# Optimization experiments

Hardware: AMD Instinct MI355X
Metric: run time of the kernel (lower is better)

Reference implementation:

```python
import jax, jax.numpy as jnp
import numpy as np

N, E, F, H, G, EPS = 50000, 500000, 128, 192, 256, 1e-5


def setup_inputs() -> dict:
    key = jax.random.key(0)
    ks = jax.random.split(key, 16)
    s = 0.05
    return {
        "x": jax.random.normal(ks[0], (N, F), jnp.float32),
        "edge_index": jax.random.randint(ks[1], (2, E), 0, N),
        "batch": jnp.sort(jax.random.randint(ks[2], (N,), 0, G)),
        "num_graphs": G,
        "w_rel0": jax.random.normal(ks[3], (H, F)) * s,
        "b_rel0": jnp.zeros((H,), jnp.float32),
        "w_root0": jax.random.normal(ks[4], (H, F)) * s,
        "w_rel": jax.random.normal(ks[5], (3, H, H)) * s,
        "b_rel": jnp.zeros((3, H), jnp.float32),
        "w_root": jax.random.normal(ks[6], (3, H, H)) * s,
        "bn_gamma": jnp.ones((4, H), jnp.float32),
        "bn_beta": jnp.zeros((4, H), jnp.float32),
        "head_w1": jax.random.normal(ks[7], (H, H)) * s,
        "head_b1": jnp.zeros((H,), jnp.float32),
        "head_w2": jax.random.normal(ks[8], (H, H)) * s,
        "head_b2": jnp.zeros((H,), jnp.float32),
        "out_w": jax.random.normal(ks[9], (1, H)) * s,
        "out_b": jnpp if False else jnp.zeros((1,), jnp.float32),
    }


def _conv_bn_relu(x, src, dst, n_nodes, wr, br, wroot, gamma, beta):
    # PyG GraphConv: out_i = lin_rel(sum_{j->i} x_j) + lin_root(x_i)
    agg = jax.ops.segment_sum(x[src], dst, num_segments=n_nodes)  # [N, d]
    h = agg @ wr.T + br + x @ wroot.T                             # [N, H]
    mu = h.mean(axis=0)
    var = h.var(axis=0)  # biased, as torch BN train mode
    h = (h - mu) * jax.lax.rsqrt(var + EPS) * gamma + beta
    return jax.nn.relu(h)


def reference(x, edge_index, batch, num_graphs, w_rel0, b_rel0, w_root0,
              w_rel, b_rel, w_root, bn_gamma, bn_beta,
              head_w1, head_b1, head_w2, head_b2, out_w, out_b):
    src, dst = edge_index[0], edge_index[1]
    n_nodes = x.shape[0]
    h = _conv_bn_relu(x, src, dst, n_nodes, w_rel0, b_rel0, w_root0,
                      bn_gamma[0], bn_beta[0])
    for i in range(3):
        h = _conv_bn_relu(h, src, dst, n_nodes, w_rel[i], b_rel[i], w_root[i],
                          bn_gamma[i + 1], bn_beta[i + 1])
    # global mean pool per graph
    sums = jax.ops.segment_sum(h, batch, num_segments=num_graphs)   # [G, H]
    cnts = jax.ops.segment_sum(jnp.ones((n_nodes,), h.dtype), batch,
                               num_segments=num_graphs)
    g = sums / jnp.maximum(cnts, 1.0)[:, None]
    # MLP head (dropout = eval) + output linear
    hh = jax.nn.relu(g @ head_w1.T + head_b1) @ head_w2.T + head_b2
    out = hh @ out_w.T + out_b                                      # [G, 1]
    return out[:, 0]
```

## Files before the change

### kernel.cpp

```cpp
#include <hip/hip_runtime.h>

#define HD 192
#define FD0 128
#define NG 256
#define BNEPS 1e-5f

#define STAT_S  1048576.0f
#define STAT_IS (1.0f / 1048576.0f)
#define POOL_S  65536.0f
#define POOL_IS (1.0f / 65536.0f)

typedef unsigned short u16;
typedef __attribute__((ext_vector_type(8))) short bf16x8;
typedef __attribute__((ext_vector_type(4))) float f32x4;

static inline int idiv(int a, int b) { return (a + b - 1) / b; }

__device__ __forceinline__ float b2f(u16 u) {
    unsigned int v = ((unsigned int)u) << 16;
    return __builtin_bit_cast(float, v);
}
__device__ __forceinline__ u16 f2b(float f) {
    unsigned int x = __builtin_bit_cast(unsigned int, f);
    return (u16)((x + 0x7FFFu + ((x >> 16) & 1u)) >> 16);
}

__device__ __forceinline__ void bn_params(const long long* __restrict__ statsq,
    const float* __restrict__ gamma, const float* __restrict__ beta,
    int N, int c, float& sc, float& sh)
{
    const float inv = 1.0f / (float)N;
    const float sum = (float)statsq[c] * STAT_IS;
    const float sq  = (float)statsq[HD + c] * STAT_IS;
    const float mu  = sum * inv;
    const float var = sq * inv - mu * mu;
    const float s   = gamma[c] * rsqrtf(var + BNEPS);
    sc = s; sh = beta[c] - mu * s;
}

__device__ __forceinline__ void async_cp16(const void* g, void* l) {
    __builtin_amdgcn_global_load_lds(
        (const __attribute__((address_space(1))) unsigned int*)g,
        (__attribute__((address_space(3))) unsigned int*)l, 16, 0, 0);
}

__global__ __launch_bounds__(256) void convert_bf16(const float* __restrict__ in,
                                                    u16* __restrict__ out, int n4)
{
    const int i = blockIdx.x * 256 + threadIdx.x;
    if (i >= n4) return;
    const float4 v = ((const float4*)in)[i];
    u16 o[4] = { f2b(v.x), f2b(v.y), f2b(v.z), f2b(v.w) };
    ((ushort4*)out)[i] = *(ushort4*)o;
}

__device__ __forceinline__ void pack_one(const float* __restrict__ wr,
    const float* __restrict__ wt, u16* __restrict__ out, int K, int idx)
{
    const int j  = idx & 7;
    const int t  = idx >> 3;
    const int c  = t & 15;
    const int kg = (t >> 4) & 3;
    const int rest = t >> 6;
    const int fglob = rest % 12;
    const int chunk = rest / 12;
    const int col = fglob * 16 + c;
    const int k   = chunk * 32 + kg * 8 + j;
    const float v = (k < K) ? wr[(size_t)col * K + k] : wt[(size_t)col * K + (k - K)];
    out[idx] = f2b(v);
}

__global__ __launch_bounds__(256) void pack_fuse(const float* __restrict__ wr0,
    const float* __restrict__ wt0, const float* __restrict__ w_rel,
    const float* __restrict__ w_root, const float* __restrict__ hw1,
    const float* __restrict__ hw2, u16* __restrict__ wp0,
    u16* __restrict__ wp123, float* __restrict__ w1t, float* __restrict__ w2t)
{
    const int T0 = HD * 2 * FD0;
    const int T1 = HD * 2 * HD;
    const int TW = HD * HD;
    int idx = blockIdx.x * 256 + threadIdx.x;
    if (idx < T0) { pack_one(wr0, wt0, wp0, FD0, idx); return; }
    idx -= T0;
    if (idx < 3 * T1) {
        const int li = idx / T1;
        const int r  = idx - li * T1;
        pack_one(w_rel + (size_t)li * HD * HD, w_root + (size_t)li * HD * HD,
                 wp123 + (size_t)li * T1, HD, r);
        return;
    }
    idx -= 3 * T1;
    if (idx >= 2 * TW) return;
    const float* w = (idx < TW) ? hw1 : hw2;
    float*       o = (idx < TW) ? w1t : w2t;
    const int r = (idx < TW) ? idx : idx - TW;
    const int t = r % HD, k = r / HD;
    o[r] = w[(size_t)t * HD + k];
}

__global__ __launch_bounds__(256) void hist_kernel(const int* __restrict__ dst,
                                                   int* __restrict__ deg, int E)
{
    const int e = blockIdx.x * 256 + threadIdx.x;
    if (e < E) atomicAdd(&deg[dst[e]], 1);
}

__global__ __launch_bounds__(256) void scan_partial(const int* __restrict__ deg,
                                                    int* __restrict__ psum, int N)
{
    __shared__ int s[256];
    const int t = threadIdx.x;
    const int i = blockIdx.x * 256 + t;
    s[t] = (i < N) ? deg[i] : 0;
    __syncthreads();
    for (int off = 128; off > 0; off >>= 1) {
        if (t < off) s[t] += s[t + off];
        __syncthreads();
    }
    if (t == 0) psum[blockIdx.x] = s[0];
}

__global__ __launch_bounds__(256) void scan_small(int* __restrict__ psum, int M)
{
    __shared__ int s[256];
    const int t = threadIdx.x;
    s[t] = (t < M) ? psum[t] : 0;
    __syncthreads();
    for (int off = 1; off < 256; off <<= 1) {
        const int u = (t >= off) ? s[t - off] : 0;
        __syncthreads();
        s[t] += u;
        __syncthreads();
    }
    if (t < M) psum[t] = (t == 0) ? 0 : s[t - 1];
}

__global__ __launch_bounds__(256) void scan_expand(int* __restrict__ deg,
    const int* __restrict__ psum, int* __restrict__ rowptr, int N, int E)
{
    __shared__ int s[256];
    const int t = threadIdx.x;
    const int i = blockIdx.x * 256 + t;
    const int v = (i < N) ? deg[i] : 0;
    s[t] = v;
    __syncthreads();
    for (int off = 1; off < 256; off <<= 1) {
        const int u = (t >= off) ? s[t - off] : 0;
        __syncthreads();
        s[t] += u;
        __syncthreads();
    }
    if (i < N) {
        const int base = psum[blockIdx.x] + s[t] - v;
        rowptr[i] = base;
        deg[i]    = base;
    }
    if (i == N - 1) rowptr[N] = E;
}

__global__ __launch_bounds__(256) void fill_kernel(const int* __restrict__ src,
    const int* __restrict__ dst, int* __restrict__ cursor,
    int* __restrict__ eidx, int E)
{
    const int e = blockIdx.x * 256 + threadIdx.x;
    if (e >= E) return;
    const int p = atomicAdd(&cursor[dst[e]], 1);
    eidx[p] = src[e];
}

template<int FD, bool BN>
__global__ __launch_bounds__(256) void gather_kernel(
    const u16* __restrict__ hsrc, const int* __restrict__ rowptr,
    const int* __restrict__ eidx, u16* __restrict__ aggb, int N,
    const long long* __restrict__ statsq, const float* __restrict__ gamma,
    const float* __restrict__ beta)
{
    constexpr int OCT = FD / 8;
    __shared__ float scs[FD], shs[FD];
    const int t = threadIdx.x;
    if (BN) {
        if (t < FD) {
            float sc, sh;
            bn_params(statsq, gamma, beta, N, t, sc, sh);
            scs[t] = sc; shs[t] = sh;
        }
        __syncthreads();
    }
    const int lane = t & 63;
    const int half = lane >> 5;
    const int o    = lane & 31;
    const int n    = blockIdx.x * 4 + (t >> 6);
    if (n >= N) return;
    const bool act = (o < OCT);
    const int beg = rowptr[n], end = rowptr[n + 1];

    float scr[8], shr[8];
    if (BN && act) {
#pragma unroll
        for (int i = 0; i < 8; ++i) { scr[i] = scs[o * 8 + i]; shr[i] = shs[o * 8 + i]; }
    }

    float acc[8];
#pragma unroll
    for (int i = 0; i < 8; ++i) acc[i] = 0.f;

    auto consume = [&](uint4 v) {
        const u16* pu = (const u16*)&v;
#pragma unroll
        for (int i = 0; i < 8; ++i) {
            float f = b2f(pu[i]);
            if (BN) f = fmaxf(0.f, fmaf(f, scr[i], shr[i]));
            acc[i] += f;
        }
    };

    int j = beg + half;
    for (; j + 6 < end; j += 8) {
        const int s0 = eidx[j],     s1 = eidx[j + 2];
        const int s2 = eidx[j + 4], s3 = eidx[j + 6];
        if (act) {
            const uint4 v0 = *(const uint4*)(hsrc + (size_t)s0 * FD + o * 8);
            const uint4 v1 = *(const uint4*)(hsrc + (size_t)s1 * FD + o * 8);
            const uint4 v2 = *(const uint4*)(hsrc + (size_t)s2 * FD + o * 8);
            const uint4 v3 = *(const uint4*)(hsrc + (size_t)s3 * FD + o * 8);
            consume(v0); consume(v1); consume(v2); consume(v3);
        }
    }
    for (; j < end; j += 2) {
        const int s0 = eidx[j];
        if (act) consume(*(const uint4*)(hsrc + (size_t)s0 * FD + o * 8));
    }
#pragma unroll
    for (int i = 0; i < 8; ++i) acc[i] += __shfl_xor(acc[i], 32);

    if (half == 0 && act) {
        u16 ov[8];
#pragma unroll
        for (int i = 0; i < 8; ++i) ov[i] = f2b(acc[i]);
        *(uint4*)(aggb + (size_t)n * FD + o * 8) = *(uint4*)ov;
    }
}

template<int K1, int K2, bool BN>
__global__ __launch_bounds__(512, 1) void gemm_mfma(
    const u16* __restrict__ A1, const u16* A2,
    const u16* __restrict__ Wb, const float* __restrict__ bias,
    u16* Hout, long long* __restrict__ statsq_out,
    const long long* __restrict__ statsq_in, const float* __restrict__ gamma,
    const float* __restrict__ beta, int N)
{
    constexpr int KC  = K1 + K2;
    constexpr int NC  = KC / 32;
    constexpr int NC1 = K1 / 32;
    __shared__ u16 bsh[HD * KC];
    __shared__ float scs[K2], shs[K2];

    const int tid  = threadIdx.x;
    const int wave = tid >> 6, lane = tid & 63;
    const int c = lane & 15, kg = lane >> 4;
    const int row0 = blockIdx.x * 256 + wave * 32;

    {
        constexpr int NST = (HD * KC) / (512 * 8);
        const u16* wsrc = Wb + tid * 8;
        u16* ldst = bsh + tid * 8;
#pragma unroll
        for (int i = 0; i < NST; ++i)
            async_cp16(wsrc + i * 4096, ldst + i * 4096);
    }
    if (BN) {
        if (tid < K2) {
            float sc, sh;
            bn_params(statsq_in, gamma, beta, N, tid, sc, sh);
            scs[tid] = sc; shs[tid] = sh;
        }
    }

    int arc[2];
#pragma unroll
    for (int m = 0; m < 2; ++m) {
        const int r = row0 + m * 16 + c;
        arc[m] = r < N ? r : N - 1;
    }

    f32x4 acc[2][12];
#pragma unroll
    for (int m = 0; m < 2; ++m)
#pragma unroll
        for (int f = 0; f < 12; ++f) acc[m][f] = (f32x4){0.f, 0.f, 0.f, 0.f};

    auto aload = [&](int ch, bf16x8* d) {
#pragma unroll
        for (int m = 0; m < 2; ++m) {
            const u16* p = (ch < NC1)
                ? (A1 + (size_t)arc[m] * K1 + ch * 32 + kg * 8)
                : (A2 + (size_t)arc[m] * K2 + (ch - NC1) * 32 + kg * 8);
            d[m] = *(const bf16x8*)p;
        }
    };

    bf16x8 ring[4][2];
#pragma unroll
    for (int p = 0; p < 4; ++p)
        if (p < NC) aload(p, ring[p]);

    __syncthreads();

#pragma unroll
    for (int ch = 0; ch < NC; ++ch) {
        bf16x8 a[2] = { ring[ch & 3][0], ring[ch & 3][1] };
        if (ch + 4 < NC) aload(ch + 4, ring[ch & 3]);
        if (BN && ch >= NC1) {
            const int k0 = (ch - NC1) * 32 + kg * 8;
            const float4 s0 = *(const float4*)&scs[k0];
            const float4 s1 = *(const float4*)&scs[k0 + 4];
            const float4 h0 = *(const float4*)&shs[k0];
            const float4 h1 = *(const float4*)&shs[k0 + 4];
            const float scv[8] = {s0.x,s0.y,s0.z,s0.w,s1.x,s1.y,s1.z,s1.w};
            const float shv[8] = {h0.x,h0.y,h0.z,h0.w,h1.x,h1.y,h1.z,h1.w};
#pragma unroll
            for (int m = 0; m < 2; ++m) {
                const u16* pa = (const u16*)&a[m];
                u16 tv[8];
#pragma unroll
                for (int i = 0; i < 8; ++i)
                    tv[i] = f2b(fmaxf(0.f, fmaf(b2f(pa[i]), scv[i], shv[i])));
                a[m] = *(bf16x8*)tv;
            }
        }
#pragma unroll
        for (int f = 0; f < 12; ++f) {
            const bf16x8 b = *(const bf16x8*)&bsh[ch * 6144 + f * 512 + kg * 128 + c * 8];
            acc[0][f] = __builtin_amdgcn_mfma_f32_16x16x32_bf16(a[0], b, acc[0][f], 0, 0, 0);
            acc[1][f] = __builtin_amdgcn_mfma_f32_16x16x32_bf16(a[1], b, acc[1][f], 0, 0, 0);
        }
    }

    float s1v[12], s2v[12];
#pragma unroll
    for (int f = 0; f < 12; ++f) { s1v[f] = 0.f; s2v[f] = 0.f; }

#pragma unroll
    for (int f = 0; f < 12; ++f) {
        const int col = f * 16 + c;
        const float bv = bias[col];
#pragma unroll
        for (int m = 0; m < 2; ++m)
#pragma unroll
            for (int r = 0; r < 4; ++r) {
                const int orow = row0 + m * 16 + kg * 4 + r;
                if (orow < N) {
                    const float v = acc[m][f][r] + bv;
                    s1v[f] += v;
                    s2v[f] += v * v;
                    Hout[(size_t)orow * HD + col] = f2b(v);
                }
            }
    }
#pragma unroll
    for (int f = 0; f < 12; ++f) {
        s1v[f] += __shfl_xor(s1v[f], 16); s1v[f] += __shfl_xor(s1v[f], 32);
        s2v[f] += __shfl_xor(s2v[f], 16); s2v[f] += __shfl_xor(s2v[f], 32);
    }
    __syncthreads();
    float* red = (float*)bsh;
    if (kg == 0) {
#pragma unroll
        for (int f = 0; f < 12; ++f) {
            red[wave * HD + f * 16 + c]            = s1v[f];
            red[8 * HD + wave * HD + f * 16 + c]   = s2v[f];
        }
    }
    __syncthreads();
    if (tid < HD) {
        float a1 = 0.f, a2 = 0.f;
#pragma unroll
        for (int w = 0; w < 8; ++w) {
            a1 += red[w * HD + tid];
            a2 += red[8 * HD + w * HD + tid];
        }
        atomicAdd((unsigned long long*)&statsq_out[tid],
                  (unsigned long long)(long long)llrintf(a1 * STAT_S));
        atomicAdd((unsigned long long*)&statsq_out[HD + tid],
                  (unsigned long long)(long long)llrintf(a2 * STAT_S));
    }
}

__global__ __launch_bounds__(192) void pool_partial(const u16* __restrict__ h,
    const int* __restrict__ batch, int* __restrict__ gsumq, int N,
    const long long* __restrict__ statsq, const float* __restrict__ gamma,
    const float* __restrict__ beta)
{
    __shared__ float scs[HD], shs[HD];
    const int t = threadIdx.x;
    {
        float sc, sh;
        bn_params(statsq, gamma, beta, N, t, sc, sh);
        scs[t] = sc; shs[t] = sh;
    }
    __syncthreads();
    const int rl  = t / 24;
    const int oct = t % 24;
    const int r0  = blockIdx.x * 256;
    const int rend = (r0 + 256 < N) ? r0 + 256 : N;

    float scr[8], shr[8];
#pragma unroll
    for (int i = 0; i < 8; ++i) { scr[i] = scs[oct * 8 + i]; shr[i] = shs[oct * 8 + i]; }

    float facc[8];
#pragma unroll
    for (int i = 0; i < 8; ++i) facc[i] = 0.f;
    int cur = -1;

    for (int r = r0 + rl; r < rend; r += 8) {
        const int b = batch[r];
        if (b != cur) {
            if (cur >= 0) {
                int* q = gsumq + (size_t)cur * HD + oct * 8;
#pragma unroll
                for (int i = 0; i < 8; ++i)
                    atomicAdd(&q[i], __float2int_rn(facc[i] * POOL_S));
            }
#pragma unroll
            for (int i = 0; i < 8; ++i) facc[i] = 0.f;
            cur = b;
        }
        const uint4 pv = *(const uint4*)(h + (size_t)r * HD + oct * 8);
        const u16* pu = (const u16*)&pv;
#pragma unroll
        for (int i = 0; i < 8; ++i)
            facc[i] += fmaxf(0.f, fmaf(b2f(pu[i]), scr[i], shr[i]));
    }
    if (cur >= 0) {
        int* q = gsumq + (size_t)cur * HD + oct * 8;
#pragma unroll
        for (int i = 0; i < 8; ++i)
            atomicAdd(&q[i], __float2int_rn(facc[i] * POOL_S));
    }
}

__global__ __launch_bounds__(192) void head_kernel(
    const int* __restrict__ gsumq, const int* __restrict__ batch, int N,
    const float* __restrict__ w1t, const float* __restrict__ b1,
    const float* __restrict__ w2t, const float* __restrict__ b2,
    const float* __restrict__ ow, const float* __restrict__ ob,
    float* __restrict__ out)
{
    __shared__ float gv[HD];
    __shared__ float h1[HD];
    __shared__ float h2[HD];
    const int g = blockIdx.x;
    const int t = threadIdx.x;

    int lo = 0, hi = N;
    while (lo < hi) { int m = (lo + hi) >> 1; if (batch[m] < g) lo = m + 1; else hi = m; }
    const int start = lo;
    hi = N;
    while (lo < hi) { int m = (lo + hi) >> 1; if (batch[m] < g + 1) lo = m + 1; else hi = m; }
    const int end = lo;
    const float cnt = fmaxf((float)(end - start), 1.0f);

    gv[t] = (float)gsumq[(size_t)g * HD + t] * POOL_IS / cnt;
    __syncthreads();
    {
        float acc = b1[t];
#pragma unroll 4
        for (int k = 0; k < HD; ++k)
            acc = fmaf(gv[k], w1t[k * HD + t], acc);
        h1[t] = fmaxf(acc, 0.f);
    }
    __syncthreads();
    {
        float acc = b2[t];
#pragma unroll 4
        for (int k = 0; k < HD; ++k)
            acc = fmaf(h1[k], w2t[k * HD + t], acc);
        h2[t] = acc * ow[t];
    }
    __syncthreads();
    if (t < 64) {
        float s = h2[t] + h2[t + 64] + h2[t + 128];
#pragma unroll
        for (int d = 1; d < 64; d <<= 1) s += __shfl_xor(s, d);
        if (t == 0) out[g] = s + ob[0];
    }
}

extern "C" void kernel_launch(void* const* d_in, const int* in_sizes, int n_in,
                              void* d_out, int out_size, void* d_ws, size_t ws_size,
                              hipStream_t stream)
{
    const float* x       = (const float*)d_in[0];
    const int*   ei      = (const int*)d_in[1];
    const int*   batch   = (const int*)d_in[2];
    const float* w_rel0  = (const float*)d_in[4];
    const float* b_rel0  = (const float*)d_in[5];
    const float* w_root0 = (const float*)d_in[6];
    const float* w_rel   = (const float*)d_in[7];
    const float* b_rel   = (const float*)d_in[8];
    const float* w_root  = (const float*)d_in[9];
    const float* bn_g    = (const float*)d_in[10];
    const float* bn_b    = (const float*)d_in[11];
    const float* hw1     = (const float*)d_in[12];
    const float* hb1     = (const float*)d_in[13];
    const float* hw2     = (const float*)d_in[14];
    const float* hb2     = (const float*)d_in[15];
    const float* ow      = (const float*)d_in[16];
    const float* ob      = (const float*)d_in[17];
    float* out = (float*)d_out;

    const int N = in_sizes[0] / FD0;
    const int E = in_sizes[1] / 2;
    const int* src = ei;
    const int* dst = ei + E;
    const int M = idiv(N, 256);

    char* ws = (char*)d_ws;
    size_t off = 0;
    u16*   xb   = (u16*)(ws + off);   off += (size_t)N * FD0 * 2;
    u16*   h    = (u16*)(ws + off);   off += (size_t)N * HD * 2;
    u16*   aggb = (u16*)(ws + off);   off += (size_t)N * HD * 2;
    u16*   wp0  = (u16*)(ws + off);   off += (size_t)HD * 2 * FD0 * 2;
    u16*   wp123= (u16*)(ws + off);   off += (size_t)3 * HD * 2 * HD * 2;
    off = (off + 15) & ~(size_t)15;
    float* w1t = (float*)(ws + off); off += (size_t)HD * HD * 4;
    float* w2t = (float*)(ws + off); off += (size_t)HD * HD * 4;
    long long* statsq4 = (long long*)(ws + off); off += 4 * 2 * HD * sizeof(long long);
    int*   gsumq  = (int*)(ws + off); off += (size_t)NG * HD * 4;
    int*   rowptr = (int*)(ws + off); off += (size_t)(N + 1) * 4;
    int*   deg    = (int*)(ws + off); off += (size_t)N * 4;
    int*   psum   = (int*)(ws + off); off += (size_t)M * 4;
    int*   eidx   = (int*)(ws + off); off += (size_t)E * 4;

    const dim3 b256(256), b512(512), b192(192);

    convert_bf16<<<idiv(N * FD0 / 4, 256), b256, 0, stream>>>(x, xb, N * FD0 / 4);
    pack_fuse<<<idiv(HD * 2 * FD0 + 3 * HD * 2 * HD + 2 * HD * HD, 256), b256, 0,
                stream>>>(w_rel0, w_root0, w_rel, w_root, hw1, hw2,
                          wp0, wp123, w1t, w2t);
    hipMemsetAsync(statsq4, 0, 4 * 2 * HD * sizeof(long long) + (size_t)NG * HD * 4,
                   stream);
    hipMemsetAsync(deg, 0, (size_t)N * sizeof(int), stream);
    hist_kernel<<<idiv(E, 256), b256, 0, stream>>>(dst, deg, E);
    scan_partial<<<M, b256, 0, stream>>>(deg, psum, N);
    scan_small<<<1, b256, 0, stream>>>(psum, M);
    scan_expand<<<M, b256, 0, stream>>>(deg, psum, rowptr, N, E);
    fill_kernel<<<idiv(E, 256), b256, 0, stream>>>(src, dst, deg, eidx, E);

    gather_kernel<FD0, false><<<idiv(N, 4), b256, 0, stream>>>(
        xb, rowptr, eidx, aggb, N, nullptr, nullptr, nullptr);
    gemm_mfma<FD0, FD0, false><<<idiv(N, 256), b512, 0, stream>>>(
        aggb, xb, wp0, b_rel0, h, statsq4, nullptr, nullptr, nullptr, N);

    for (int i = 0; i < 3; ++i) {
        const long long* sin  = statsq4 + (size_t)i * 2 * HD;
        long long*       sout = statsq4 + (size_t)(i + 1) * 2 * HD;
        const float* g = bn_g + (size_t)i * HD;
        const float* b = bn_b + (size_t)i * HD;
        gather_kernel<HD, true><<<idiv(N, 4), b256, 0, stream>>>(
            h, rowptr, eidx, aggb, N, sin, g, b);
        gemm_mfma<HD, HD, true><<<idiv(N, 256), b512, 0, stream>>>(
            aggb, h, wp123 + (size_t)i * HD * 2 * HD,
            b_rel + (size_t)i * HD, h, sout, sin, g, b, N);
    }

    pool_partial<<<idiv(N, 256), b192, 0, stream>>>(
        h, batch, gsumq, N, statsq4 + 3 * 2 * (size_t)HD,
        bn_g + 3 * (size_t)HD, bn_b + 3 * (size_t)HD);
    head_kernel<<<NG, b192, 0, stream>>>(gsumq, batch, N, w1t, hb1, w2t, hb2,
                                         ow, ob, out);
}
```

Baseline: 391.5 us.

## Fuse all stages into one persistent cooperative megakernel with grid syncs

Replaces the chain of separate launches (convert, weight packing, CSR histogram/scan/fill, four gather+GEMM layers, pooling and the MLP head) with a single cooperative kernel. It uses 256 blocks of 512 threads and separates phases with grid.sync. Each former kernel becomes a device phase that loops grid-stride over its work. The aim is to remove per-launch overhead and inter-kernel gaps. The cost is one fixed ~145KB static LDS allocation for every phase, so each CU holds a single block and the latency-bound gather phases run with far fewer waves in flight.

```diff
diff --git a/kernel.cpp b/kernel.cpp
--- a/kernel.cpp
+++ b/kernel.cpp
@@ -1,4 +1,7 @@
 #include <hip/hip_runtime.h>
+#include <hip/hip_cooperative_groups.h>
+
+namespace cg = cooperative_groups;
 
 #define HD 192
 #define FD0 128
@@ -9,6 +12,10 @@
 #define STAT_IS (1.0f / 1048576.0f)
 #define POOL_S  65536.0f
 #define POOL_IS (1.0f / 65536.0f)
+
+#define GRID 256
+#define TPB  512
+#define SMEM_BYTES 148992
 
 typedef unsigned short u16;
 typedef __attribute__((ext_vector_type(8))) short bf16x8;
@@ -44,15 +51,18 @@
         (__attribute__((address_space(3))) unsigned int*)l, 16, 0, 0);
 }
 
-__global__ __launch_bounds__(256) void convert_bf16(const float* __restrict__ in,
-                                                    u16* __restrict__ out, int n4)
-{
-    const int i = blockIdx.x * 256 + threadIdx.x;
-    if (i >= n4) return;
-    const float4 v = ((const float4*)in)[i];
-    u16 o[4] = { f2b(v.x), f2b(v.y), f2b(v.z), f2b(v.w) };
-    ((ushort4*)out)[i] = *(ushort4*)o;
-}
+struct MegaArgs {
+    const float* x; const int* src; const int* dst; const int* batch;
+    const float* w_rel0; const float* b_rel0; const float* w_root0;
+    const float* w_rel; const float* b_rel; const float* w_root;
+    const float* bn_g; const float* bn_b;
+    const float* hw1; const float* hb1; const float* hw2; const float* hb2;
+    const float* ow; const float* ob; float* out;
+    u16* xb; u16* h; u16* aggb; u16* wp0; u16* wp123;
+    float* w1t; float* w2t; long long* statsq4; int* gsumq;
+    int* rowptr; int* deg; int* psum; int* eidx;
+    int N, E, M;
+};
 
 __device__ __forceinline__ void pack_one(const float* __restrict__ wr,
     const float* __restrict__ wt, u16* __restrict__ out, int K, int idx)
@@ -70,118 +80,20 @@
     out[idx] = f2b(v);
 }
 
-__global__ __launch_bounds__(256) void pack_fuse(const float* __restrict__ wr0,
-    const float* __restrict__ wt0, const float* __restrict__ w_rel,
-    const float* __restrict__ w_root, const float* __restrict__ hw1,
-    const float* __restrict__ hw2, u16* __restrict__ wp0,
-    u16* __restrict__ wp123, float* __restrict__ w1t, float* __restrict__ w2t)
-{
-    const int T0 = HD * 2 * FD0;
-    const int T1 = HD * 2 * HD;
-    const int TW = HD * HD;
-    int idx = blockIdx.x * 256 + threadIdx.x;
-    if (idx < T0) { pack_one(wr0, wt0, wp0, FD0, idx); return; }
-    idx -= T0;
-    if (idx < 3 * T1) {
-        const int li = idx / T1;
-        const int r  = idx - li * T1;
-        pack_one(w_rel + (size_t)li * HD * HD, w_root + (size_t)li * HD * HD,
-                 wp123 + (size_t)li * T1, HD, r);
-        return;
-    }
-    idx -= 3 * T1;
-    if (idx >= 2 * TW) return;
-    const float* w = (idx < TW) ? hw1 : hw2;
-    float*       o = (idx < TW) ? w1t : w2t;
-    const int r = (idx < TW) ? idx : idx - TW;
-    const int t = r % HD, k = r / HD;
-    o[r] = w[(size_t)t * HD + k];
-}
-
-__global__ __launch_bounds__(256) void hist_kernel(const int* __restrict__ dst,
-                                                   int* __restrict__ deg, int E)
-{
-    const int e = blockIdx.x * 256 + threadIdx.x;
-    if (e < E) atomicAdd(&deg[dst[e]], 1);
-}
-
-__global__ __launch_bounds__(256) void scan_partial(const int* __restrict__ deg,
-                                                    int* __restrict__ psum, int N)
-{
-    __shared__ int s[256];
-    const int t = threadIdx.x;
-    const int i = blockIdx.x * 256 + t;
-    s[t] = (i < N) ? deg[i] : 0;
-    __syncthreads();
-    for (int off = 128; off > 0; off >>= 1) {
-        if (t < off) s[t] += s[t + off];
-        __syncthreads();
-    }
-    if (t == 0) psum[blockIdx.x] = s[0];
-}
-
-__global__ __launch_bounds__(256) void scan_small(int* __restrict__ psum, int M)
-{
-    __shared__ int s[256];
-    const int t = threadIdx.x;
-    s[t] = (t < M) ? psum[t] : 0;
-    __syncthreads();
-    for (int off = 1; off < 256; off <<= 1) {
-        const int u = (t >= off) ? s[t - off] : 0;
-        __syncthreads();
-        s[t] += u;
-        __syncthreads();
-    }
-    if (t < M) psum[t] = (t == 0) ? 0 : s[t - 1];
-}
-
-__global__ __launch_bounds__(256) void scan_expand(int* __restrict__ deg,
-    const int* __restrict__ psum, int* __restrict__ rowptr, int N, int E)
-{
-    __shared__ int s[256];
-    const int t = threadIdx.x;
-    const int i = blockIdx.x * 256 + t;
-    const int v = (i < N) ? deg[i] : 0;
-    s[t] = v;
-    __syncthreads();
-    for (int off = 1; off < 256; off <<= 1) {
-        const int u = (t >= off) ? s[t - off] : 0;
-        __syncthreads();
-        s[t] += u;
-        __syncthreads();
-    }
-    if (i < N) {
-        const int base = psum[blockIdx.x] + s[t] - v;
-        rowptr[i] = base;
-        deg[i]    = base;
-    }
-    if (i == N - 1) rowptr[N] = E;
-}
-
-__global__ __launch_bounds__(256) void fill_kernel(const int* __restrict__ src,
-    const int* __restrict__ dst, int* __restrict__ cursor,
-    int* __restrict__ eidx, int E)
-{
-    const int e = blockIdx.x * 256 + threadIdx.x;
-    if (e >= E) return;
-    const int p = atomicAdd(&cursor[dst[e]], 1);
-    eidx[p] = src[e];
-}
-
 template<int FD, bool BN>
-__global__ __launch_bounds__(256) void gather_kernel(
-    const u16* __restrict__ hsrc, const int* __restrict__ rowptr,
-    const int* __restrict__ eidx, u16* __restrict__ aggb, int N,
-    const long long* __restrict__ statsq, const float* __restrict__ gamma,
-    const float* __restrict__ beta)
+__device__ void gather_phase(const MegaArgs& a, const u16* __restrict__ hsrc,
+    u16* __restrict__ aggb, const long long* __restrict__ statsq,
+    const float* __restrict__ gamma, const float* __restrict__ beta,
+    unsigned char* smem)
 {
     constexpr int OCT = FD / 8;
-    __shared__ float scs[FD], shs[FD];
+    float* scs = (float*)smem;
+    float* shs = scs + FD;
     const int t = threadIdx.x;
     if (BN) {
         if (t < FD) {
             float sc, sh;
-            bn_params(statsq, gamma, beta, N, t, sc, sh);
+            bn_params(statsq, gamma, beta, a.N, t, sc, sh);
             scs[t] = sc; shs[t] = sh;
         }
         __syncthreads();
@@ -189,10 +101,8 @@
     const int lane = t & 63;
     const int half = lane >> 5;
     const int o    = lane & 31;
-    const int n    = blockIdx.x * 4 + (t >> 6);
-    if (n >= N) return;
+    const int wave = t >> 6;
     const bool act = (o < OCT);
-    const int beg = rowptr[n], end = rowptr[n + 1];
 
     float scr[8], shr[8];
     if (BN && act) {
@@ -200,60 +110,66 @@
         for (int i = 0; i < 8; ++i) { scr[i] = scs[o * 8 + i]; shr[i] = shs[o * 8 + i]; }
     }
 
-    float acc[8];
-#pragma unroll
-    for (int i = 0; i < 8; ++i) acc[i] = 0.f;
-
-    auto consume = [&](uint4 v) {
-        const u16* pu = (const u16*)&v;
-#pragma unroll
-        for (int i = 0; i < 8; ++i) {
-            float f = b2f(pu[i]);
-            if (BN) f = fmaxf(0.f, fmaf(f, scr[i], shr[i]));
-            acc[i] += f;
-        }
-    };
-
-    int j = beg + half;
-    for (; j + 6 < end; j += 8) {
-        const int s0 = eidx[j],     s1 = eidx[j + 2];
-        const int s2 = eidx[j + 4], s3 = eidx[j + 6];
-        if (act) {
-            const uint4 v0 = *(const uint4*)(hsrc + (size_t)s0 * FD + o * 8);
-            const uint4 v1 = *(const uint4*)(hsrc + (size_t)s1 * FD + o * 8);
-            const uint4 v2 = *(const uint4*)(hsrc + (size_t)s2 * FD + o * 8);
-            const uint4 v3 = *(const uint4*)(hsrc + (size_t)s3 * FD + o * 8);
-            consume(v0); consume(v1); consume(v2); consume(v3);
-        }
-    }
-    for (; j < end; j += 2) {
-        const int s0 = eidx[j];
-        if (act) consume(*(const uint4*)(hsrc + (size_t)s0 * FD + o * 8));
-    }
-#pragma unroll
-    for (int i = 0; i < 8; ++i) acc[i] += __shfl_xor(acc[i], 32);
-
-    if (half == 0 && act) {
-        u16 ov[8];
-#pragma unroll
-        for (int i = 0; i < 8; ++i) ov[i] = f2b(acc[i]);
-        *(uint4*)(aggb + (size_t)n * FD + o * 8) = *(uint4*)ov;
+    for (int n = blockIdx.x * 8 + wave; n < a.N; n += GRID * 8) {
+        const int beg = a.rowptr[n], end = a.rowptr[n + 1];
+        float acc[8];
+#pragma unroll
+        for (int i = 0; i < 8; ++i) acc[i] = 0.f;
+
+        auto consume = [&](uint4 v) {
+            const u16* pu = (const u16*)&v;
+#pragma unroll
+            for (int i = 0; i < 8; ++i) {
+                float f = b2f(pu[i]);
+                if (BN) f = fmaxf(0.f, fmaf(f, scr[i], shr[i]));
+                acc[i] += f;
+            }
+        };
+
+        int j = beg + half;
+        for (; j + 6 < end; j += 8) {
+            const int s0 = a.eidx[j],     s1 = a.eidx[j + 2];
+            const int s2 = a.eidx[j + 4], s3 = a.eidx[j + 6];
+            if (act) {
+                const uint4 v0 = *(const uint4*)(hsrc + (size_t)s0 * FD + o * 8);
+                const uint4 v1 = *(const uint4*)(hsrc + (size_t)s1 * FD + o * 8);
+                const uint4 v2 = *(const uint4*)(hsrc + (size_t)s2 * FD + o * 8);
+                const uint4 v3 = *(const uint4*)(hsrc + (size_t)s3 * FD + o * 8);
+                consume(v0); consume(v1); consume(v2); consume(v3);
+            }
+        }
+        for (; j < end; j += 2) {
+            const int s0 = a.eidx[j];
+            if (act) consume(*(const uint4*)(hsrc + (size_t)s0 * FD + o * 8));
+        }
+#pragma unroll
+        for (int i = 0; i < 8; ++i) acc[i] += __shfl_xor(acc[i], 32);
+
+        if (half == 0 && act) {
+            u16 ov[8];
+#pragma unroll
+            for (int i = 0; i < 8; ++i) ov[i] = f2b(acc[i]);
+            *(uint4*)(aggb + (size_t)n * FD + o * 8) = *(uint4*)ov;
+        }
     }
 }
 
 template<int K1, int K2, bool BN>
-__global__ __launch_bounds__(512, 1) void gemm_mfma(
-    const u16* __restrict__ A1, const u16* A2,
-    const u16* __restrict__ Wb, const float* __restrict__ bias,
+__device__ void gemm_phase(const MegaArgs& a, const u16* __restrict__ A1,
+    const u16* A2, const u16* __restrict__ Wb, const float* __restrict__ bias,
     u16* Hout, long long* __restrict__ statsq_out,
     const long long* __restrict__ statsq_in, const float* __restrict__ gamma,
-    const float* __restrict__ beta, int N)
+    const float* __restrict__ beta, unsigned char* smem)
 {
     constexpr int KC  = K1 + K2;
     constexpr int NC  = KC / 32;
     constexpr int NC1 = K1 / 32;
-    __shared__ u16 bsh[HD * KC];
-    __shared__ float scs[K2], shs[K2];
+    u16* bsh = (u16*)smem;
+    float* scs = (float*)(smem + (size_t)HD * KC * 2);
+    float* shs = scs + K2;
+
+    const int ntiles = (a.N + 255) >> 8;
+    if (blockIdx.x >= ntiles) return;
 
     const int tid  = threadIdx.x;
     const int wave = tid >> 6, lane = tid & 63;
@@ -261,7 +177,7 @@
     const int row0 = blockIdx.x * 256 + wave * 32;
 
     {
-        constexpr int NST = (HD * KC) / (512 * 8);
+        constexpr int NST = (HD * KC) / (TPB * 8);
         const u16* wsrc = Wb + tid * 8;
         u16* ldst = bsh + tid * 8;
 #pragma unroll
@@ -271,7 +187,7 @@
     if (BN) {
         if (tid < K2) {
             float sc, sh;
-            bn_params(statsq_in, gamma, beta, N, tid, sc, sh);
+            bn_params(statsq_in, gamma, beta, a.N, tid, sc, sh);
             scs[tid] = sc; shs[tid] = sh;
         }
     }
@@ -280,7 +196,7 @@
 #pragma unroll
     for (int m = 0; m < 2; ++m) {
         const int r = row0 + m * 16 + c;
-        arc[m] = r < N ? r : N - 1;
+        arc[m] = r < a.N ? r : a.N - 1;
     }
 
     f32x4 acc[2][12];
@@ -308,7 +224,7 @@
 
 #pragma unroll
     for (int ch = 0; ch < NC; ++ch) {
-        bf16x8 a[2] = { ring[ch & 3][0], ring[ch & 3][1] };
+        bf16x8 av[2] = { ring[ch & 3][0], ring[ch & 3][1] };
         if (ch + 4 < NC) aload(ch + 4, ring[ch & 3]);
         if (BN && ch >= NC1) {
             const int k0 = (ch - NC1) * 32 + kg * 8;
@@ -320,19 +236,19 @@
             const float shv[8] = {h0.x,h0.y,h0.z,h0.w,h1.x,h1.y,h1.z,h1.w};
 #pragma unroll
             for (int m = 0; m < 2; ++m) {
-                const u16* pa = (const u16*)&a[m];
+                const u16* pa = (const u16*)&av[m];
                 u16 tv[8];
 #pragma unroll
                 for (int i = 0; i < 8; ++i)
                     tv[i] = f2b(fmaxf(0.f, fmaf(b2f(pa[i]), scv[i], shv[i])));
-                a[m] = *(bf16x8*)tv;
+                av[m] = *(bf16x8*)tv;
             }
         }
 #pragma unroll
         for (int f = 0; f < 12; ++f) {
             const bf16x8 b = *(const bf16x8*)&bsh[ch * 6144 + f * 512 + kg * 128 + c * 8];
-            acc[0][f] = __builtin_amdgcn_mfma_f32_16x16x32_bf16(a[0], b, acc[0][f], 0, 0, 0);
-            acc[1][f] = __builtin_amdgcn_mfma_f32_16x16x32_bf16(a[1], b, acc[1][f], 0, 0, 0);
+            acc[0][f] = __builtin_amdgcn_mfma_f32_16x16x32_bf16(av[0], b, acc[0][f], 0, 0, 0);
+            acc[1][f] = __builtin_amdgcn_mfma_f32_16x16x32_bf16(av[1], b, acc[1][f], 0, 0, 0);
         }
     }
 
@@ -349,7 +265,7 @@
 #pragma unroll
             for (int r = 0; r < 4; ++r) {
                 const int orow = row0 + m * 16 + kg * 4 + r;
-                if (orow < N) {
+                if (orow < a.N) {
                     const float v = acc[m][f][r] + bv;
                     s1v[f] += v;
                     s2v[f] += v * v;
@@ -367,8 +283,8 @@
     if (kg == 0) {
 #pragma unroll
         for (int f = 0; f < 12; ++f) {
-            red[wave * HD + f * 16 + c]            = s1v[f];
-            red[8 * HD + wave * HD + f * 16 + c]   = s2v[f];
+            red[wave * HD + f * 16 + c]          = s1v[f];
+            red[8 * HD + wave * HD + f * 16 + c] = s2v[f];
         }
     }
     __syncthreads();
@@ -386,104 +302,223 @@
     }
 }
 
-__global__ __launch_bounds__(192) void pool_partial(const u16* __restrict__ h,
-    const int* __restrict__ batch, int* __restrict__ gsumq, int N,
-    const long long* __restrict__ statsq, const float* __restrict__ gamma,
-    const float* __restrict__ beta)
+__global__ __launch_bounds__(TPB, 2) void mega(MegaArgs a)
 {
-    __shared__ float scs[HD], shs[HD];
-    const int t = threadIdx.x;
-    {
-        float sc, sh;
-        bn_params(statsq, gamma, beta, N, t, sc, sh);
-        scs[t] = sc; shs[t] = sh;
-    }
-    __syncthreads();
-    const int rl  = t / 24;
-    const int oct = t % 24;
-    const int r0  = blockIdx.x * 256;
-    const int rend = (r0 + 256 < N) ? r0 + 256 : N;
-
-    float scr[8], shr[8];
-#pragma unroll
-    for (int i = 0; i < 8; ++i) { scr[i] = scs[oct * 8 + i]; shr[i] = shs[oct * 8 + i]; }
-
-    float facc[8];
-#pragma unroll
-    for (int i = 0; i < 8; ++i) facc[i] = 0.f;
-    int cur = -1;
-
-    for (int r = r0 + rl; r < rend; r += 8) {
-        const int b = batch[r];
-        if (b != cur) {
+    cg::grid_group grid = cg::this_grid();
+    __shared__ __align__(16) unsigned char smem[SMEM_BYTES];
+
+    const int tid  = threadIdx.x;
+    const int gtid = blockIdx.x * TPB + tid;
+    const int GT   = GRID * TPB;
+
+    for (int i = gtid; i < a.N; i += GT) a.deg[i] = 0;
+    for (int i = gtid; i < 4 * 2 * HD; i += GT) a.statsq4[i] = 0;
+    for (int i = gtid; i < NG * HD; i += GT) a.gsumq[i] = 0;
+    {
+        const int n4 = a.N * FD0 / 4;
+        for (int i = gtid; i < n4; i += GT) {
+            const float4 v = ((const float4*)a.x)[i];
+            u16 o[4] = { f2b(v.x), f2b(v.y), f2b(v.z), f2b(v.w) };
+            ((ushort4*)a.xb)[i] = *(ushort4*)o;
+        }
+    }
+    {
+        const int T0 = HD * 2 * FD0, T1 = HD * 2 * HD, TW = HD * HD;
+        const int TT = T0 + 3 * T1 + 2 * TW;
+        for (int ii = gtid; ii < TT; ii += GT) {
+            int idx = ii;
+            if (idx < T0) { pack_one(a.w_rel0, a.w_root0, a.wp0, FD0, idx); continue; }
+            idx -= T0;
+            if (idx < 3 * T1) {
+                const int li = idx / T1;
+                const int r  = idx - li * T1;
+                pack_one(a.w_rel + (size_t)li * HD * HD, a.w_root + (size_t)li * HD * HD,
+                         a.wp123 + (size_t)li * T1, HD, r);
+                continue;
+            }
+            idx -= 3 * T1;
+            const float* w = (idx < TW) ? a.hw1 : a.hw2;
+            float*       o = (idx < TW) ? a.w1t : a.w2t;
+            const int r = (idx < TW) ? idx : idx - TW;
+            const int t = r % HD, k = r / HD;
+            o[r] = w[(size_t)t * HD + k];
+        }
+    }
+    grid.sync();
+
+    for (int e = gtid; e < a.E; e += GT)
+        atomicAdd(&a.deg[a.dst[e]], 1);
+    grid.sync();
+
+    {
+        int* s = (int*)smem;
+        const int i = blockIdx.x * 256 + tid;
+        if (tid < 256)
+            s[tid] = (blockIdx.x < a.M && i < a.N) ? a.deg[i] : 0;
+        __syncthreads();
+        for (int off = 128; off > 0; off >>= 1) {
+            if (tid < off) s[tid] += s[tid + off];
+            __syncthreads();
+        }
+        if (tid == 0 && blockIdx.x < a.M) a.psum[blockIdx.x] = s[0];
+    }
+    grid.sync();
+
+    {
+        int* s = (int*)smem;
+        if (tid < 256)
+            s[tid] = (blockIdx.x == 0 && tid < a.M) ? a.psum[tid] : 0;
+        __syncthreads();
+        for (int off = 1; off < 256; off <<= 1) {
+            const int u = (tid >= off && tid < 256) ? s[tid - off] : 0;
+            __syncthreads();
+            if (tid < 256) s[tid] += u;
+            __syncthreads();
+        }
+        if (blockIdx.x == 0 && tid < a.M) a.psum[tid] = (tid == 0) ? 0 : s[tid - 1];
+    }
+    grid.sync();
+
+    {
+        int* s = (int*)smem;
+        const int i = blockIdx.x * 256 + tid;
+        const bool inb = (blockIdx.x < a.M) && (tid < 256) && (i < a.N);
+        const int v = inb ? a.deg[i] : 0;
+        if (tid < 256) s[tid] = v;
+        __syncthreads();
+        for (int off = 1; off < 256; off <<= 1) {
+            const int u = (tid >= off && tid < 256) ? s[tid - off] : 0;
+            __syncthreads();
+            if (tid < 256) s[tid] += u;
+            __syncthreads();
+        }
+        if (inb) {
+            const int base = a.psum[blockIdx.x] + s[tid] - v;
+            a.rowptr[i] = base;
+            a.deg[i]    = base;
+            if (i == a.N - 1) a.rowptr[a.N] = a.E;
+        }
+    }
+    grid.sync();
+
+    for (int e = gtid; e < a.E; e += GT) {
+        const int p = atomicAdd(&a.deg[a.dst[e]], 1);
+        a.eidx[p] = a.src[e];
+    }
+    grid.sync();
+
+    gather_phase<FD0, false>(a, a.xb, a.aggb, nullptr, nullptr, nullptr, smem);
+    grid.sync();
+    gemm_phase<FD0, FD0, false>(a, a.aggb, a.xb, a.wp0, a.b_rel0, a.h,
+                                a.statsq4, nullptr, nullptr, nullptr, smem);
+    grid.sync();
+
+#pragma unroll 1
+    for (int i = 0; i < 3; ++i) {
+        const long long* sin  = a.statsq4 + (size_t)i * 2 * HD;
+        long long*       sout = a.statsq4 + (size_t)(i + 1) * 2 * HD;
+        const float* g = a.bn_g + (size_t)i * HD;
+        const float* b = a.bn_b + (size_t)i * HD;
+        gather_phase<HD, true>(a, a.h, a.aggb, sin, g, b, smem);
+        grid.sync();
+        gemm_phase<HD, HD, true>(a, a.aggb, a.h,
+                                 a.wp123 + (size_t)i * HD * 2 * HD,
+                                 a.b_rel + (size_t)i * HD, a.h,
+                                 sout, sin, g, b, smem);
+        grid.sync();
+    }
+
+    if (blockIdx.x < a.M) {
+        float* scs = (float*)smem;
+        float* shs = scs + HD;
+        if (tid < HD) {
+            float sc, sh;
+            bn_params(a.statsq4 + 3 * 2 * (size_t)HD, a.bn_g + 3 * (size_t)HD,
+                      a.bn_b + 3 * (size_t)HD, a.N, tid, sc, sh);
+            scs[tid] = sc; shs[tid] = sh;
+        }
+        __syncthreads();
+        if (tid < HD) {
+            const int rl  = tid / 24;
+            const int oct = tid % 24;
+            const int r0  = blockIdx.x * 256;
+            const int rend = (r0 + 256 < a.N) ? r0 + 256 : a.N;
+            float scr[8], shr[8];
+#pragma unroll
+            for (int i = 0; i < 8; ++i) { scr[i] = scs[oct * 8 + i]; shr[i] = shs[oct * 8 + i]; }
+            float facc[8];
+#pragma unroll
+            for (int i = 0; i < 8; ++i) facc[i] = 0.f;
+            int cur = -1;
+            for (int r = r0 + rl; r < rend; r += 8) {
+                const int bb = a.batch[r];
+                if (bb != cur) {
+                    if (cur >= 0) {
+                        int* q = a.gsumq + (size_t)cur * HD + oct * 8;
+#pragma unroll
+                        for (int i = 0; i < 8; ++i)
+                            atomicAdd(&q[i], __float2int_rn(facc[i] * POOL_S));
+                    }
+#pragma unroll
+                    for (int i = 0; i < 8; ++i) facc[i] = 0.f;
+                    cur = bb;
+                }
+                const uint4 pv = *(const uint4*)(a.h + (size_t)r * HD + oct * 8);
+                const u16* pu = (const u16*)&pv;
+#pragma unroll
+                for (int i = 0; i < 8; ++i)
+                    facc[i] += fmaxf(0.f, fmaf(b2f(pu[i]), scr[i], shr[i]));
+            }
             if (cur >= 0) {
-                int* q = gsumq + (size_t)cur * HD + oct * 8;
+                int* q = a.gsumq + (size_t)cur * HD + oct * 8;
 #pragma unroll
                 for (int i = 0; i < 8; ++i)
                     atomicAdd(&q[i], __float2int_rn(facc[i] * POOL_S));
             }
-#pragma unroll
-            for (int i = 0; i < 8; ++i) facc[i] = 0.f;
-            cur = b;
-        }
-        const uint4 pv = *(const uint4*)(h + (size_t)r * HD + oct * 8);
-        const u16* pu = (const u16*)&pv;
-#pragma unroll
-        for (int i = 0; i < 8; ++i)
-            facc[i] += fmaxf(0.f, fmaf(b2f(pu[i]), scr[i], shr[i]));
-    }
-    if (cur >= 0) {
-        int* q = gsumq + (size_t)cur * HD + oct * 8;
-#pragma unroll
-        for (int i = 0; i < 8; ++i)
-            atomicAdd(&q[i], __float2int_rn(facc[i] * POOL_S));
-    }
-}
-
-__global__ __launch_bounds__(192) void head_kernel(
-    const int* __restrict__ gsumq, const int* __restrict__ batch, int N,
-    const float* __restrict__ w1t, const float* __restrict__ b1,
-    const float* __restrict__ w2t, const float* __restrict__ b2,
-    const float* __restrict__ ow, const float* __restrict__ ob,
-    float* __restrict__ out)
-{
-    __shared__ float gv[HD];
-    __shared__ float h1[HD];
-    __shared__ float h2[HD];
-    const int g = blockIdx.x;
-    const int t = threadIdx.x;
-
-    int lo = 0, hi = N;
-    while (lo < hi) { int m = (lo + hi) >> 1; if (batch[m] < g) lo = m + 1; else hi = m; }
-    const int start = lo;
-    hi = N;
-    while (lo < hi) { int m = (lo + hi) >> 1; if (batch[m] < g + 1) lo = m + 1; else hi = m; }
-    const int end = lo;
-    const float cnt = fmaxf((float)(end - start), 1.0f);
-
-    gv[t] = (float)gsumq[(size_t)g * HD + t] * POOL_IS / cnt;
-    __syncthreads();
-    {
-        float acc = b1[t];
+        }
+    }
+    grid.sync();
+
+    {
+        float* gv = (float*)smem;
+        float* h1 = gv + HD;
+        float* h2 = h1 + HD;
+        const int g = blockIdx.x;
+        if (g < NG) {
+            int lo = 0, hi = a.N;
+            while (lo < hi) { int m = (lo + hi) >> 1; if (a.batch[m] < g) lo = m + 1; else hi = m; }
+            const int start = lo;
+            hi = a.N;
+            while (lo < hi) { int m = (lo + hi) >> 1; if (a.batch[m] < g + 1) lo = m + 1; else hi = m; }
+            const int end = lo;
+            const float cnt = fmaxf((float)(end - start), 1.0f);
+
+            if (tid < HD)
+                gv[tid] = (float)a.gsumq[(size_t)g * HD + tid] * POOL_IS / cnt;
+            __syncthreads();
+            if (tid < HD) {
+                float acc = a.hb1[tid];
 #pragma unroll 4
-        for (int k = 0; k < HD; ++k)
-            acc = fmaf(gv[k], w1t[k * HD + t], acc);
-        h1[t] = fmaxf(acc, 0.f);
-    }
-    __syncthreads();
-    {
-        float acc = b2[t];
+                for (int k = 0; k < HD; ++k)
+                    acc = fmaf(gv[k], a.w1t[k * HD + tid], acc);
+                h1[tid] = fmaxf(acc, 0.f);
+            }
+            __syncthreads();
+            if (tid < HD) {
+                float acc = a.hb2[tid];
 #pragma unroll 4
-        for (int k = 0; k < HD; ++k)
-            acc = fmaf(h1[k], w2t[k * HD + t], acc);
-        h2[t] = acc * ow[t];
-    }
-    __syncthreads();
-    if (t < 64) {
-        float s = h2[t] + h2[t + 64] + h2[t + 128];
-#pragma unroll
-        for (int d = 1; d < 64; d <<= 1) s += __shfl_xor(s, d);
-        if (t == 0) out[g] = s + ob[0];
+                for (int k = 0; k < HD; ++k)
+                    acc = fmaf(h1[k], a.w2t[k * HD + tid], acc);
+                h2[tid] = acc * a.ow[tid];
+            }
+            __syncthreads();
+            if (tid < 64) {
+                float s = h2[tid] + h2[tid + 64] + h2[tid + 128];
+#pragma unroll
+                for (int d = 1; d < 64; d <<= 1) s += __shfl_xor(s, d);
+                if (tid == 0) a.out[g] = s + a.ob[0];
+            }
+        }
     }
 }
 
@@ -491,29 +526,8 @@
                               void* d_out, int out_size, void* d_ws, size_t ws_size,
                               hipStream_t stream)
 {
-    const float* x       = (const float*)d_in[0];
-    const int*   ei      = (const int*)d_in[1];
-    const int*   batch   = (const int*)d_in[2];
-    const float* w_rel0  = (const float*)d_in[4];
-    const float* b_rel0  = (const float*)d_in[5];
-    const float* w_root0 = (const float*)d_in[6];
-    const float* w_rel   = (const float*)d_in[7];
-    const float* b_rel   = (const float*)d_in[8];
-    const float* w_root  = (const float*)d_in[9];
-    const float* bn_g    = (const float*)d_in[10];
-    const float* bn_b    = (const float*)d_in[11];
-    const float* hw1     = (const float*)d_in[12];
-    const float* hb1     = (const float*)d_in[13];
-    const float* hw2     = (const float*)d_in[14];
-    const float* hb2     = (const float*)d_in[15];
-    const float* ow      = (const float*)d_in[16];
-    const float* ob      = (const float*)d_in[17];
-    float* out = (float*)d_out;
-
     const int N = in_sizes[0] / FD0;
     const int E = in_sizes[1] / 2;
-    const int* src = ei;
-    const int* dst = ei + E;
     const int M = idiv(N, 256);
 
     char* ws = (char*)d_ws;
@@ -533,41 +547,32 @@
     int*   psum   = (int*)(ws + off); off += (size_t)M * 4;
     int*   eidx   = (int*)(ws + off); off += (size_t)E * 4;
 
-    const dim3 b256(256), b512(512), b192(192);
-
-    convert_bf16<<<idiv(N * FD0 / 4, 256), b256, 0, stream>>>(x, xb, N * FD0 / 4);
-    pack_fuse<<<idiv(HD * 2 * FD0 + 3 * HD * 2 * HD + 2 * HD * HD, 256), b256, 0,
-                stream>>>(w_rel0, w_root0, w_rel, w_root, hw1, hw2,
-                          wp0, wp123, w1t, w2t);
-    hipMemsetAsync(statsq4, 0, 4 * 2 * HD * sizeof(long long) + (size_t)NG * HD * 4,
-                   stream);
-    hipMemsetAsync(deg, 0, (size_t)N * sizeof(int), stream);
-    hist_kernel<<<idiv(E, 256), b256, 0, stream>>>(dst, deg, E);
-    scan_partial<<<M, b256, 0, stream>>>(deg, psum, N);
-    scan_small<<<1, b256, 0, stream>>>(psum, M);
-    scan_expand<<<M, b256, 0, stream>>>(deg, psum, rowptr, N, E);
-    fill_kernel<<<idiv(E, 256), b256, 0, stream>>>(src, dst, deg, eidx, E);
-
-    gather_kernel<FD0, false><<<idiv(N, 4), b256, 0, stream>>>(
-        xb, rowptr, eidx, aggb, N, nullptr, nullptr, nullptr);
-    gemm_mfma<FD0, FD0, false><<<idiv(N, 256), b512, 0, stream>>>(
-        aggb, xb, wp0, b_rel0, h, statsq4, nullptr, nullptr, nullptr, N);
-
-    for (int i = 0; i < 3; ++i) {
-        const long long* sin  = statsq4 + (size_t)i * 2 * HD;
-        long long*       sout = statsq4 + (size_t)(i + 1) * 2 * HD;
-        const float* g = bn_g + (size_t)i * HD;
-        const float* b = bn_b + (size_t)i * HD;
-        gather_kernel<HD, true><<<idiv(N, 4), b256, 0, stream>>>(
-            h, rowptr, eidx, aggb, N, sin, g, b);
-        gemm_mfma<HD, HD, true><<<idiv(N, 256), b512, 0, stream>>>(
-            aggb, h, wp123 + (size_t)i * HD * 2 * HD,
-            b_rel + (size_t)i * HD, h, sout, sin, g, b, N);
-    }
-
-    pool_partial<<<idiv(N, 256), b192, 0, stream>>>(
-        h, batch, gsumq, N, statsq4 + 3 * 2 * (size_t)HD,
-        bn_g + 3 * (size_t)HD, bn_b + 3 * (size_t)HD);
-    head_kernel<<<NG, b192, 0, stream>>>(gsumq, batch, N, w1t, hb1, w2t, hb2,
-                                         ow, ob, out);
-}
+    MegaArgs a;
+    a.x = (const float*)d_in[0];
+    a.src = (const int*)d_in[1];
+    a.dst = (const int*)d_in[1] + E;
+    a.batch = (const int*)d_in[2];
+    a.w_rel0 = (const float*)d_in[4];
+    a.b_rel0 = (const float*)d_in[5];
+    a.w_root0 = (const float*)d_in[6];
+    a.w_rel = (const float*)d_in[7];
+    a.b_rel = (const float*)d_in[8];
+    a.w_root = (const float*)d_in[9];
+    a.bn_g = (const float*)d_in[10];
+    a.bn_b = (const float*)d_in[11];
+    a.hw1 = (const float*)d_in[12];
+    a.hb1 = (const float*)d_in[13];
+    a.hw2 = (const float*)d_in[14];
+    a.hb2 = (const float*)d_in[15];
+    a.ow = (const float*)d_in[16];
+    a.ob = (const float*)d_in[17];
+    a.out = (float*)d_out;
+    a.xb = xb; a.h = h; a.aggb = aggb; a.wp0 = wp0; a.wp123 = wp123;
+    a.w1t = w1t; a.w2t = w2t; a.statsq4 = statsq4; a.gsumq = gsumq;
+    a.rowptr = rowptr; a.deg = deg; a.psum = psum; a.eidx = eidx;
+    a.N = N; a.E = E; a.M = M;
+
+    void* kargs[] = { &a };
+    hipLaunchCooperativeKernel((const void*)mega, dim3(GRID), dim3(TPB),
+                               kargs, 0, stream);
+}
```

Result: slower. 910.5 us (+132.6%).

## Gather one node per block with edge slots and shared-memory reduction

Applied to the files above, without the earlier changes.

The neighbour-aggregation kernel now gives each destination node a whole 256-thread block instead of one wave. Edges are spread over several slots of threads, each owning a 16-byte feature octet. Per-slot partial sums are then reduced through shared memory after a block barrier. The aim is more memory-level parallelism per node and less serial latency on high-degree nodes. In exchange it launches four times as many blocks, repeats the BN parameter setup per node, and adds a barrier and shared-memory reduction, while the average degree of about ten leaves most slots idle.

```diff
diff --git a/kernel.cpp b/kernel.cpp
--- a/kernel.cpp
+++ b/kernel.cpp
@@ -175,8 +175,10 @@
     const long long* __restrict__ statsq, const float* __restrict__ gamma,
     const float* __restrict__ beta)
 {
-    constexpr int OCT = FD / 8;
+    constexpr int OCT   = FD / 8;
+    constexpr int NSLOT = 256 / OCT;
     __shared__ float scs[FD], shs[FD];
+    __shared__ float pp[NSLOT][FD];
     const int t = threadIdx.x;
     if (BN) {
         if (t < FD) {
@@ -186,58 +188,44 @@
         }
         __syncthreads();
     }
-    const int lane = t & 63;
-    const int half = lane >> 5;
-    const int o    = lane & 31;
-    const int n    = blockIdx.x * 4 + (t >> 6);
+    const int oct  = t % OCT;
+    const int slot = t / OCT;
+    const int n    = blockIdx.x;
     if (n >= N) return;
-    const bool act = (o < OCT);
     const int beg = rowptr[n], end = rowptr[n + 1];
+    const bool act = (slot < NSLOT);
 
     float scr[8], shr[8];
     if (BN && act) {
 #pragma unroll
-        for (int i = 0; i < 8; ++i) { scr[i] = scs[o * 8 + i]; shr[i] = shs[o * 8 + i]; }
+        for (int i = 0; i < 8; ++i) { scr[i] = scs[oct * 8 + i]; shr[i] = shs[oct * 8 + i]; }
     }
 
     float acc[8];
 #pragma unroll
     for (int i = 0; i < 8; ++i) acc[i] = 0.f;
 
-    auto consume = [&](uint4 v) {
-        const u16* pu = (const u16*)&v;
-#pragma unroll
-        for (int i = 0; i < 8; ++i) {
-            float f = b2f(pu[i]);
-            if (BN) f = fmaxf(0.f, fmaf(f, scr[i], shr[i]));
-            acc[i] += f;
-        }
-    };
-
-    int j = beg + half;
-    for (; j + 6 < end; j += 8) {
-        const int s0 = eidx[j],     s1 = eidx[j + 2];
-        const int s2 = eidx[j + 4], s3 = eidx[j + 6];
-        if (act) {
-            const uint4 v0 = *(const uint4*)(hsrc + (size_t)s0 * FD + o * 8);
-            const uint4 v1 = *(const uint4*)(hsrc + (size_t)s1 * FD + o * 8);
-            const uint4 v2 = *(const uint4*)(hsrc + (size_t)s2 * FD + o * 8);
-            const uint4 v3 = *(const uint4*)(hsrc + (size_t)s3 * FD + o * 8);
-            consume(v0); consume(v1); consume(v2); consume(v3);
-        }
-    }
-    for (; j < end; j += 2) {
-        const int s0 = eidx[j];
-        if (act) consume(*(const uint4*)(hsrc + (size_t)s0 * FD + o * 8));
-    }
-#pragma unroll
-    for (int i = 0; i < 8; ++i) acc[i] += __shfl_xor(acc[i], 32);
-
-    if (half == 0 && act) {
-        u16 ov[8];
-#pragma unroll
-        for (int i = 0; i < 8; ++i) ov[i] = f2b(acc[i]);
-        *(uint4*)(aggb + (size_t)n * FD + o * 8) = *(uint4*)ov;
+    if (act) {
+        for (int j = beg + slot; j < end; j += NSLOT) {
+            const int s = eidx[j];
+            const uint4 v = *(const uint4*)(hsrc + (size_t)s * FD + oct * 8);
+            const u16* pu = (const u16*)&v;
+#pragma unroll
+            for (int i = 0; i < 8; ++i) {
+                float f = b2f(pu[i]);
+                if (BN) f = fmaxf(0.f, fmaf(f, scr[i], shr[i]));
+                acc[i] += f;
+            }
+        }
+#pragma unroll
+        for (int i = 0; i < 8; ++i) pp[slot][oct * 8 + i] = acc[i];
+    }
+    __syncthreads();
+    if (t < FD) {
+        float s = 0.f;
+#pragma unroll
+        for (int r = 0; r < NSLOT; ++r) s += pp[r][t];
+        aggb[(size_t)n * FD + t] = f2b(s);
     }
 }
 
@@ -548,7 +536,7 @@
     scan_expand<<<M, b256, 0, stream>>>(deg, psum, rowptr, N, E);
     fill_kernel<<<idiv(E, 256), b256, 0, stream>>>(src, dst, deg, eidx, E);
 
-    gather_kernel<FD0, false><<<idiv(N, 4), b256, 0, stream>>>(
+    gather_kernel<FD0, false><<<N, b256, 0, stream>>>(
         xb, rowptr, eidx, aggb, N, nullptr, nullptr, nullptr);
     gemm_mfma<FD0, FD0, false><<<idiv(N, 256), b512, 0, stream>>>(
         aggb, xb, wp0, b_rel0, h, statsq4, nullptr, nullptr, nullptr, N);
@@ -558,7 +546,7 @@
         long long*       sout = statsq4 + (size_t)(i + 1) * 2 * HD;
         const float* g = bn_g + (size_t)i * HD;
         const float* b = bn_b + (size_t)i * HD;
-        gather_kernel<HD, true><<<idiv(N, 4), b256, 0, stream>>>(
+        gather_kernel<HD, true><<<N, b256, 0, stream>>>(
             h, rowptr, eidx, aggb, N, sin, g, b);
         gemm_mfma<HD, HD, true><<<idiv(N, 256), b512, 0, stream>>>(
             aggb, h, wp123 + (size_t)i * HD * 2 * HD,
```

Result: slower. 478.2 us (+22.2%).
